# Kernel tuning notes

Hardware: AMD Instinct MI355X
Metric: run time of the kernel (lower is better)

Reference implementation:

```python
import jax, jax.numpy as jnp
import numpy as np

B, N, C, H, S = 8, 1024, 768, 8, 16  # C = 3 * S * S, head_dim = C // H
NCH = 3
D = C // H
SCALE = D ** -0.5
REATTEN_SCALE = 1.0  # transform_scale=False
EPS = 1e-5  # BatchNorm2d eps


def conv3x3(x, w, b):
    # x: (B*N, 3, S, S); w: (O=3, I=3, 3, 3) OIHW; 'same' padding
    y = jax.lax.conv_general_dilated(x, w, (1, 1), 'SAME',
                                     dimension_numbers=('NCHW', 'OIHW', 'NCHW'))
    return y + b[None, :, None, None]


def setup_inputs() -> dict:
    key = jax.random.key(0)
    ks = jax.random.split(key, 8)
    return {
        'x': jax.random.normal(ks[0], (B, N, C), jnp.float32),
        'qw': jax.random.normal(ks[1], (NCH, NCH, 3, 3), jnp.float32) * 0.1,
        'qb': jnp.zeros((NCH,), jnp.float32),
        'kw': jax.random.normal(ks[2], (NCH, NCH, 3, 3), jnp.float32) * 0.1,
        'kb': jnp.zeros((NCH,), jnp.float32),
        'vw': jax.random.normal(ks[3], (NCH, NCH, 3, 3), jnp.float32) * 0.1,
        'vb': jnp.zeros((NCH,), jnp.float32),
        'rw': jax.random.normal(ks[4], (H, H), jnp.float32) * 0.2,  # 1x1 conv over heads
        'rb': jnp.zeros((H,), jnp.float32),
        'bn_g': jnp.ones((H,), jnp.float32),
        'bn_b': jnp.zeros((H,), jnp.float32),
        'bn_m': jnp.zeros((H,), jnp.float32),   # running mean
        'bn_v': jnp.ones((H,), jnp.float32),    # running var
        'pw': jax.random.normal(ks[5], (C, C), jnp.float32) * 0.02,
        'pb': jnp.zeros((C,), jnp.float32),
    }


def reference(x, qw, qb, kw, kb, vw, vb, rw, rb, bn_g, bn_b, bn_m, bn_v, pw, pb):
    Bx, Nx, Cx = x.shape
    xs = x.reshape(Bx * Nx, NCH, S, S)  # unflatten; all (b, n) convs batched at once

    def heads(y):  # (B*N, 3, S, S) -> (B, H, N, D)
        return y.reshape(Bx, Nx, H, D).transpose(0, 2, 1, 3)

    q = heads(conv3x3(xs, qw, qb))
    k = heads(conv3x3(xs, kw, kb))
    v = heads(conv3x3(xs, vw, vb))

    attn = jnp.einsum('bhnd,bhmd->bhnm', q, k) * SCALE  # (B, H, N, N)
    attn = jax.nn.softmax(attn, axis=-1)
    # re-attention: 1x1 conv across heads, then BatchNorm2d (eval, running stats)
    attn = jnp.einsum('oh,bhnm->bonm', rw, attn) + rb[None, :, None, None]
    inv = (bn_g / jnp.sqrt(bn_v + EPS))[None, :, None, None]
    attn = (attn - bn_m[None, :, None, None]) * inv + bn_b[None, :, None, None]
    attn = attn * REATTEN_SCALE

    out = jnp.einsum('bhnm,bhmd->bhnd', attn, v)  # (B, H, N, D)
    out = out.transpose(0, 2, 1, 3).reshape(Bx, Nx, Cx)
    out = out @ pw.T + pb
    return (out, attn)
```

## Files before the change

kernel.cpp:

```cpp
#include <hip/hip_runtime.h>
#include <math.h>

#define B_ 8
#define N_ 1024
#define C_ 768
#define H_ 8
#define D_ 96
#define SCALE_F 0.1020620726159657f

typedef unsigned short u16;
typedef __bf16 bf16x8 __attribute__((ext_vector_type(8)));
typedef float f32x4 __attribute__((ext_vector_type(4)));

#define MFMA(a, b, c) __builtin_amdgcn_mfma_f32_16x16x32_bf16(a, b, c, 0, 0, 0)

__device__ inline void split1(float x, u16& h, u16& l) {
    __bf16 hb = (__bf16)x;
    float hf = (float)hb;
    __bf16 lb = (__bf16)(x - hf);
    h = __builtin_bit_cast(u16, hb);
    l = __builtin_bit_cast(u16, lb);
}

__device__ inline void split4(float4 x, ushort4& h, ushort4& l) {
    split1(x.x, h.x, l.x);
    split1(x.y, h.y, l.y);
    split1(x.z, h.z, l.z);
    split1(x.w, h.w, l.w);
}

__device__ inline void bar_lds() {
    asm volatile("s_waitcnt lgkmcnt(0)" ::: "memory");
    __builtin_amdgcn_s_barrier();
}

__global__ __launch_bounds__(256) void conv_qkv(
    const float* __restrict__ x,
    const float* __restrict__ qw, const float* __restrict__ qb,
    const float* __restrict__ kw, const float* __restrict__ kb,
    const float* __restrict__ vw, const float* __restrict__ vb,
    u16* __restrict__ qh, u16* __restrict__ ql,
    u16* __restrict__ kh, u16* __restrict__ kl,
    float* __restrict__ v)
{
    __shared__ float simg[768];
    __shared__ float sw[243];
    __shared__ float sb[9];
    const int img = blockIdx.x;
    const int b = img >> 10;
    const int tid = threadIdx.x;

    for (int i = tid; i < 768; i += 256) simg[i] = x[(size_t)img * 768 + i];
    if (tid < 243) {
        int g = tid / 81, i = tid % 81;
        const float* w = (g == 0) ? qw : (g == 1) ? kw : vw;
        sw[tid] = w[i];
    }
    if (tid < 9) {
        int g = tid / 3, i = tid % 3;
        const float* bb = (g == 0) ? qb : (g == 1) ? kb : vb;
        sb[tid] = bb[i];
    }
    __syncthreads();

    const int n = img & 1023;
    for (int e = tid; e < 2304; e += 256) {
        int g = e / 768, c = e % 768;
        int oc = c >> 8, rem = c & 255, y = rem >> 4, xx = rem & 15;
        float acc = sb[g * 3 + oc];
        const float* wg = &sw[g * 81 + oc * 27];
        #pragma unroll
        for (int ic = 0; ic < 3; ++ic)
            #pragma unroll
            for (int ky = 0; ky < 3; ++ky) {
                int yy = y + ky - 1;
                if (yy < 0 || yy > 15) continue;
                #pragma unroll
                for (int kx = 0; kx < 3; ++kx) {
                    int xp = xx + kx - 1;
                    if (xp < 0 || xp > 15) continue;
                    acc += wg[ic * 9 + ky * 3 + kx] * simg[ic * 256 + yy * 16 + xp];
                }
            }
        int hh = c / 96, d = c % 96;
        size_t o = ((size_t)(b * 8 + hh) * 1024 + n) * 96 + d;
        if (g == 2) {
            v[o] = acc;
        } else {
            u16 hi, lo;
            split1(acc, hi, lo);
            if (g == 0) { qh[o] = hi; ql[o] = lo; }
            else        { kh[o] = hi; kl[o] = lo; }
        }
    }
}

__global__ __launch_bounds__(256) void vt_split(
    const float* __restrict__ v, u16* __restrict__ vt_h)
{
    __shared__ float t32[32][36];
    const int bh = blockIdx.z, n0 = blockIdx.x * 32, d0 = blockIdx.y * 32;
    const int tid = threadIdx.x;
    {
        int nn = tid >> 3, c4 = (tid & 7) * 4;
        float4 x = *(const float4*)&v[((size_t)bh * 1024 + n0 + nn) * 96 + d0 + c4];
        t32[nn][c4] = x.x; t32[nn][c4 + 1] = x.y;
        t32[nn][c4 + 2] = x.z; t32[nn][c4 + 3] = x.w;
    }
    __syncthreads();
    {
        int d = tid >> 3, n4 = (tid & 7) * 4;
        ushort4 h;
        h.x = __builtin_bit_cast(u16, (__bf16)t32[n4][d]);
        h.y = __builtin_bit_cast(u16, (__bf16)t32[n4 + 1][d]);
        h.z = __builtin_bit_cast(u16, (__bf16)t32[n4 + 2][d]);
        h.w = __builtin_bit_cast(u16, (__bf16)t32[n4 + 3][d]);
        size_t o = ((size_t)bh * 96 + d0 + d) * 1024 + n0 + n4;
        *(ushort4*)&vt_h[o] = h;
    }
}

__global__ __launch_bounds__(256) void pw_split(
    const float* __restrict__ pw, u16* __restrict__ pwh, u16* __restrict__ pwl)
{
    int i = blockIdx.x * 256 + threadIdx.x;
    float4 x = *(const float4*)&pw[(size_t)i * 4];
    ushort4 h, l;
    split4(x, h, l);
    *(ushort4*)&pwh[(size_t)i * 4] = h;
    *(ushort4*)&pwl[(size_t)i * 4] = l;
}

__global__ __launch_bounds__(512) void fused_attn(
    const u16* __restrict__ qh, const u16* __restrict__ ql,
    const u16* __restrict__ kh, const u16* __restrict__ kl,
    const u16* __restrict__ vth,
    const float* __restrict__ rw, const float* __restrict__ rb,
    const float* __restrict__ bn_g, const float* __restrict__ bn_b,
    const float* __restrict__ bn_m, const float* __restrict__ bn_v,
    float* __restrict__ attn, u16* __restrict__ o1h, u16* __restrict__ o1l)
{
    __shared__ float p_lds[2][8][32][36];
    __shared__ float s_w2[8][8];
    __shared__ float s_b2[8];

    const int bid = blockIdx.x;
    const int b = bid & 7;
    const int n0 = (bid >> 3) * 32;
    const int tid = threadIdx.x, wid = tid >> 6, lane = tid & 63;
    const int l16 = lane & 15, kg = lane >> 4;
    const int h = wid;
    const size_t bh = (size_t)(b * 8 + h);

    if (tid < 64) {
        int o = tid >> 3, hh = tid & 7;
        float inv = bn_g[o] * rsqrtf(bn_v[o] + 1e-5f);
        s_w2[o][hh] = rw[o * 8 + hh] * inv;
        if (hh == 0) s_b2[o] = (rb[o] - bn_m[o]) * inv + bn_b[o];
    }

    bf16x8 qhf[2][3], qlf[2][3];
    #pragma unroll
    for (int nf = 0; nf < 2; ++nf)
        #pragma unroll
        for (int ks = 0; ks < 3; ++ks) {
            size_t off = (bh * 1024 + n0 + nf * 16 + l16) * 96 + ks * 32 + kg * 8;
            qhf[nf][ks] = *(const bf16x8*)&qh[off];
            qlf[nf][ks] = *(const bf16x8*)&ql[off];
        }

    float ls[2][4];
    #pragma unroll
    for (int nf = 0; nf < 2; ++nf)
        #pragma unroll
        for (int r = 0; r < 4; ++r) ls[nf][r] = 0.f;

    #pragma unroll 1
    for (int mt = 0; mt < 16; ++mt) {
        const int m0 = mt * 64;
        f32x4 sacc[2][4];
        #pragma unroll
        for (int nf = 0; nf < 2; ++nf)
            #pragma unroll
            for (int mf = 0; mf < 4; ++mf) sacc[nf][mf] = (f32x4){0.f, 0.f, 0.f, 0.f};

        __builtin_amdgcn_s_setprio(1);
        #pragma unroll
        for (int ks = 0; ks < 3; ++ks) {
            bf16x8 kbh[4];
            #pragma unroll
            for (int mf = 0; mf < 4; ++mf) {
                size_t off = (bh * 1024 + m0 + mf * 16 + l16) * 96 + ks * 32 + kg * 8;
                kbh[mf] = *(const bf16x8*)&kh[off];
            }
            #pragma unroll
            for (int nf = 0; nf < 2; ++nf)
                #pragma unroll
                for (int mf = 0; mf < 4; ++mf)
                    sacc[nf][mf] = MFMA(qhf[nf][ks], kbh[mf], sacc[nf][mf]);
        }
        __builtin_amdgcn_s_setprio(0);

        #pragma unroll
        for (int nf = 0; nf < 2; ++nf)
            #pragma unroll
            for (int mf = 0; mf < 4; ++mf)
                #pragma unroll
                for (int r = 0; r < 4; ++r)
                    ls[nf][r] += __expf(sacc[nf][mf][r] * SCALE_F);
    }

    float rv[2][4];
    #pragma unroll
    for (int nf = 0; nf < 2; ++nf)
        #pragma unroll
        for (int r = 0; r < 4; ++r) {
            float s = ls[nf][r];
            #pragma unroll
            for (int off = 1; off < 16; off <<= 1) s += __shfl_xor(s, off);
            rv[nf][r] = 1.0f / s;
        }

    __syncthreads();

    float w2r[8];
    #pragma unroll
    for (int hh = 0; hh < 8; ++hh) w2r[hh] = s_w2[h][hh];
    const float b2h = s_b2[h];

    f32x4 pvacc[2][6];
    #pragma unroll
    for (int nf = 0; nf < 2; ++nf)
        #pragma unroll
        for (int df = 0; df < 6; ++df) pvacc[nf][df] = (f32x4){0.f, 0.f, 0.f, 0.f};

#define QKEXP(MT, BUF)                                                          \
    {                                                                           \
        const int m0_ = (MT) * 32;                                              \
        f32x4 sacc_[2][2];                                                      \
        _Pragma("unroll")                                                       \
        for (int nf_ = 0; nf_ < 2; ++nf_)                                       \
            _Pragma("unroll")                                                   \
            for (int mf_ = 0; mf_ < 2; ++mf_)                                   \
                sacc_[nf_][mf_] = (f32x4){0.f, 0.f, 0.f, 0.f};                  \
        __builtin_amdgcn_s_setprio(1);                                          \
        _Pragma("unroll")                                                       \
        for (int ks_ = 0; ks_ < 3; ++ks_) {                                     \
            bf16x8 kbh_[2], kbl_[2];                                            \
            _Pragma("unroll")                                                   \
            for (int mf_ = 0; mf_ < 2; ++mf_) {                                 \
                size_t off_ = (bh * 1024 + m0_ + mf_ * 16 + l16) * 96 + ks_ * 32 + kg * 8; \
                kbh_[mf_] = *(const bf16x8*)&kh[off_];                          \
                kbl_[mf_] = *(const bf16x8*)&kl[off_];                          \
            }                                                                   \
            _Pragma("unroll")                                                   \
            for (int nf_ = 0; nf_ < 2; ++nf_)                                   \
                _Pragma("unroll")                                               \
                for (int mf_ = 0; mf_ < 2; ++mf_) {                             \
                    sacc_[nf_][mf_] = MFMA(qhf[nf_][ks_], kbh_[mf_], sacc_[nf_][mf_]); \
                    sacc_[nf_][mf_] = MFMA(qhf[nf_][ks_], kbl_[mf_], sacc_[nf_][mf_]); \
                    sacc_[nf_][mf_] = MFMA(qlf[nf_][ks_], kbh_[mf_], sacc_[nf_][mf_]); \
                }                                                               \
        }                                                                       \
        __builtin_amdgcn_s_setprio(0);                                          \
        _Pragma("unroll")                                                       \
        for (int nf_ = 0; nf_ < 2; ++nf_)                                       \
            _Pragma("unroll")                                                   \
            for (int mf_ = 0; mf_ < 2; ++mf_)                                   \
                _Pragma("unroll")                                               \
                for (int r_ = 0; r_ < 4; ++r_) {                                \
                    float pp_ = __expf(sacc_[nf_][mf_][r_] * SCALE_F) * rv[nf_][r_]; \
                    p_lds[BUF][h][nf_ * 16 + kg * 4 + r_][mf_ * 16 + l16] = pp_; \
                }                                                               \
    }

    QKEXP(0, 0)
    bar_lds();

    #pragma unroll 1
    for (int mt = 0; mt < 32; ++mt) {
        const int m0 = mt * 32;
        const int buf = mt & 1;

        bf16x8 vbh[6];
        #pragma unroll
        for (int df = 0; df < 6; ++df) {
            size_t off = (bh * 96 + df * 16 + l16) * 1024 + m0 + kg * 8;
            vbh[df] = *(const bf16x8*)&vth[off];
        }

        if (mt < 31) QKEXP(mt + 1, buf ^ 1)

        float mixf[2][8];
        #pragma unroll
        for (int nf = 0; nf < 2; ++nf)
            #pragma unroll
            for (int j = 0; j < 8; ++j) mixf[nf][j] = b2h;
        #pragma unroll
        for (int hh = 0; hh < 8; ++hh) {
            float w = w2r[hh];
            #pragma unroll
            for (int nf = 0; nf < 2; ++nf) {
                const float* pp = &p_lds[buf][hh][nf * 16 + l16][kg * 8];
                float4 a0 = *(const float4*)pp;
                float4 a1 = *(const float4*)(pp + 4);
                mixf[nf][0] += w * a0.x; mixf[nf][1] += w * a0.y;
                mixf[nf][2] += w * a0.z; mixf[nf][3] += w * a0.w;
                mixf[nf][4] += w * a1.x; mixf[nf][5] += w * a1.y;
                mixf[nf][6] += w * a1.z; mixf[nf][7] += w * a1.w;
            }
        }

        #pragma unroll
        for (int nf = 0; nf < 2; ++nf) {
            float* gp = &attn[(bh * 1024 + n0 + nf * 16 + l16) * 1024 + m0 + kg * 8];
            f32x4 v0 = {mixf[nf][0], mixf[nf][1], mixf[nf][2], mixf[nf][3]};
            f32x4 v1 = {mixf[nf][4], mixf[nf][5], mixf[nf][6], mixf[nf][7]};
            __builtin_nontemporal_store(v0, (f32x4*)gp);
            __builtin_nontemporal_store(v1, (f32x4*)(gp + 4));
        }

        bf16x8 mah[2];
        #pragma unroll
        for (int nf = 0; nf < 2; ++nf)
            #pragma unroll
            for (int j = 0; j < 8; ++j)
                mah[nf][j] = (__bf16)mixf[nf][j];
        __builtin_amdgcn_s_setprio(1);
        #pragma unroll
        for (int df = 0; df < 6; ++df)
            #pragma unroll
            for (int nf = 0; nf < 2; ++nf)
                pvacc[nf][df] = MFMA(mah[nf], vbh[df], pvacc[nf][df]);
        __builtin_amdgcn_s_setprio(0);

        bar_lds();
    }
#undef QKEXP

    #pragma unroll
    for (int nf = 0; nf < 2; ++nf)
        #pragma unroll
        for (int df = 0; df < 6; ++df)
            #pragma unroll
            for (int r = 0; r < 4; ++r) {
                int row = n0 + nf * 16 + kg * 4 + r;
                int col = h * 96 + df * 16 + l16;
                u16 hh2, ll2;
                split1(pvacc[nf][df][r], hh2, ll2);
                size_t o = ((size_t)b * 1024 + row) * 768 + col;
                o1h[o] = hh2;
                o1l[o] = ll2;
            }
}

__global__ __launch_bounds__(256) void proj_mfma(
    const u16* __restrict__ o1h, const u16* __restrict__ o1l,
    const u16* __restrict__ pwh, const u16* __restrict__ pwl,
    const float* __restrict__ pb, float* __restrict__ out)
{
    __shared__ __align__(16) u16 Ahs[5120], Als[5120];
    __shared__ __align__(16) u16 Bhs[2560], Bls[2560];
    const int t0 = blockIdx.y * 128, o0 = blockIdx.x * 64;
    const int tid = threadIdx.x;
    const int wid = tid >> 6, lane = tid & 63;
    const int l16 = lane & 15, kg = lane >> 4;
    const int wr = wid >> 1, wc = wid & 1;

    f32x4 acc[4][2];
    #pragma unroll
    for (int i = 0; i < 4; ++i)
        #pragma unroll
        for (int j = 0; j < 2; ++j) acc[i][j] = (f32x4){0.f, 0.f, 0.f, 0.f};

    for (int s = 0; s < 24; ++s) {
        const int kc = s * 32;
        if (s) __syncthreads();
        #pragma unroll
        for (int i = 0; i < 4; ++i) {
            int idx = tid + i * 256;
            int r = idx >> 3, c4 = idx & 7;
            *(ushort4*)&Ahs[r * 40 + c4 * 4] = *(const ushort4*)&o1h[(size_t)(t0 + r) * 768 + kc + c4 * 4];
            *(ushort4*)&Als[r * 40 + c4 * 4] = *(const ushort4*)&o1l[(size_t)(t0 + r) * 768 + kc + c4 * 4];
        }
        #pragma unroll
        for (int i = 0; i < 2; ++i) {
            int idx = tid + i * 256;
            int r = idx >> 3, c4 = idx & 7;
            *(ushort4*)&Bhs[r * 40 + c4 * 4] = *(const ushort4*)&pwh[(size_t)(o0 + r) * 768 + kc + c4 * 4];
            *(ushort4*)&Bls[r * 40 + c4 * 4] = *(const ushort4*)&pwl[(size_t)(o0 + r) * 768 + kc + c4 * 4];
        }
        __syncthreads();

        bf16x8 ah[4], al[4], bh8[2], bl8[2];
        #pragma unroll
        for (int f = 0; f < 4; ++f) {
            int ra = (wr * 64 + f * 16 + l16) * 40 + kg * 8;
            ah[f] = *(const bf16x8*)&Ahs[ra];
            al[f] = *(const bf16x8*)&Als[ra];
        }
        #pragma unroll
        for (int j = 0; j < 2; ++j) {
            int rb = (wc * 32 + j * 16 + l16) * 40 + kg * 8;
            bh8[j] = *(const bf16x8*)&Bhs[rb];
            bl8[j] = *(const bf16x8*)&Bls[rb];
        }
        #pragma unroll
        for (int i = 0; i < 4; ++i)
            #pragma unroll
            for (int j = 0; j < 2; ++j) {
                acc[i][j] = MFMA(ah[i], bh8[j], acc[i][j]);
                acc[i][j] = MFMA(ah[i], bl8[j], acc[i][j]);
                acc[i][j] = MFMA(al[i], bh8[j], acc[i][j]);
            }
    }

    #pragma unroll
    for (int i = 0; i < 4; ++i) {
        int rr = t0 + wr * 64 + i * 16 + kg * 4;
        #pragma unroll
        for (int j = 0; j < 2; ++j) {
            int cc = o0 + wc * 32 + j * 16 + l16;
            float bias = pb[cc];
            #pragma unroll
            for (int r = 0; r < 4; ++r)
                __builtin_nontemporal_store(acc[i][j][r] + bias,
                                            &out[(size_t)(rr + r) * 768 + cc]);
        }
    }
}

extern "C" void kernel_launch(void* const* d_in, const int* in_sizes, int n_in,
                              void* d_out, int out_size, void* d_ws, size_t ws_size,
                              hipStream_t stream)
{
    const float* x    = (const float*)d_in[0];
    const float* qw   = (const float*)d_in[1];
    const float* qb   = (const float*)d_in[2];
    const float* kw   = (const float*)d_in[3];
    const float* kb   = (const float*)d_in[4];
    const float* vw   = (const float*)d_in[5];
    const float* vb   = (const float*)d_in[6];
    const float* rw   = (const float*)d_in[7];
    const float* rb   = (const float*)d_in[8];
    const float* bn_g = (const float*)d_in[9];
    const float* bn_b = (const float*)d_in[10];
    const float* bn_m = (const float*)d_in[11];
    const float* bn_v = (const float*)d_in[12];
    const float* pw   = (const float*)d_in[13];
    const float* pb   = (const float*)d_in[14];

    float* out_p  = (float*)d_out;
    float* attn_p = out_p + (size_t)B_ * N_ * C_;

    float* ws = (float*)d_ws;
    const size_t qkv = (size_t)B_ * H_ * N_ * D_;

    float* vf  = ws;
    u16* qhp = (u16*)(ws + qkv);
    u16* qlp = qhp + qkv;
    u16* khp = qlp + qkv;
    u16* klp = khp + qkv;
    u16* vth = (u16*)(ws + 3 * qkv);
    u16* o1h = (u16*)(ws + 4 * qkv);
    u16* o1l = o1h + qkv;
    u16* pwh = (u16*)(ws + 5 * qkv);
    u16* pwl = pwh + (size_t)C_ * C_;

    conv_qkv<<<B_ * N_, 256, 0, stream>>>(x, qw, qb, kw, kb, vw, vb,
                                          qhp, qlp, khp, klp, vf);
    vt_split<<<dim3(32, 3, 64), 256, 0, stream>>>(vf, vth);
    pw_split<<<576, 256, 0, stream>>>(pw, pwh, pwl);
    fused_attn<<<256, 512, 0, stream>>>(qhp, qlp, khp, klp, vth,
                                        rw, rb, bn_g, bn_b, bn_m, bn_v,
                                        attn_p, o1h, o1l);
    proj_mfma<<<dim3(12, 64), 256, 0, stream>>>(o1h, o1l, pwh, pwl, pb, out_p);
}
```

Baseline: 294.6 us.

## Compute head-mixing once per element via bf16 head-interleaved LDS staging

Softmax probabilities are now staged in LDS as bf16 with the head index innermost. Each thread reads all 8 heads for one (n,m) position and computes all 8 mixed output heads, so each wave no longer rereads every head's 32x32 tile. The mixed values are written to the attention output with coalesced scalar stores and staged through a second bf16 LDS buffer for the PV MFMA, using a mid-iteration barrier. This cuts redundant LDS reads and halves LDS footprint per element. In exchange, probabilities are rounded to bf16 before mixing, which lowers the precision of the returned attention map, and global stores are narrower.

```diff
diff --git a/kernel.cpp b/kernel.cpp
--- a/kernel.cpp
+++ b/kernel.cpp
@@ -11,6 +11,7 @@
 typedef unsigned short u16;
 typedef __bf16 bf16x8 __attribute__((ext_vector_type(8)));
 typedef float f32x4 __attribute__((ext_vector_type(4)));
+typedef u16 u16x8 __attribute__((ext_vector_type(8)));
 
 #define MFMA(a, b, c) __builtin_amdgcn_mfma_f32_16x16x32_bf16(a, b, c, 0, 0, 0)
 
@@ -32,6 +33,10 @@
 __device__ inline void bar_lds() {
     asm volatile("s_waitcnt lgkmcnt(0)" ::: "memory");
     __builtin_amdgcn_s_barrier();
+}
+
+__device__ inline float bf16_to_f32(u16 u) {
+    return __builtin_bit_cast(float, (unsigned)u << 16);
 }
 
 __global__ __launch_bounds__(256) void conv_qkv(
@@ -140,7 +145,8 @@
     const float* __restrict__ bn_m, const float* __restrict__ bn_v,
     float* __restrict__ attn, u16* __restrict__ o1h, u16* __restrict__ o1l)
 {
-    __shared__ float p_lds[2][8][32][36];
+    __shared__ u16 p_lds[2][32][33][8];
+    __shared__ u16 m_lds[2][8][32][40];
     __shared__ float s_w2[8][8];
     __shared__ float s_b2[8];
 
@@ -223,16 +229,23 @@
 
     __syncthreads();
 
-    float w2r[8];
-    #pragma unroll
-    for (int hh = 0; hh < 8; ++hh) w2r[hh] = s_w2[h][hh];
-    const float b2h = s_b2[h];
+    float w2all[8][8], b2r[8];
+    #pragma unroll
+    for (int o = 0; o < 8; ++o) {
+        b2r[o] = s_b2[o];
+        #pragma unroll
+        for (int hh = 0; hh < 8; ++hh) w2all[o][hh] = s_w2[o][hh];
+    }
 
     f32x4 pvacc[2][6];
     #pragma unroll
     for (int nf = 0; nf < 2; ++nf)
         #pragma unroll
         for (int df = 0; df < 6; ++df) pvacc[nf][df] = (f32x4){0.f, 0.f, 0.f, 0.f};
+
+    const int mm = lane & 31, halfq = lane >> 5;
+    const int nlA = wid * 4 + halfq;
+    const int nlB = wid * 4 + 2 + halfq;
 
 #define QKEXP(MT, BUF)                                                          \
     {                                                                           \
@@ -270,7 +283,8 @@
                 _Pragma("unroll")                                               \
                 for (int r_ = 0; r_ < 4; ++r_) {                                \
                     float pp_ = __expf(sacc_[nf_][mf_][r_] * SCALE_F) * rv[nf_][r_]; \
-                    p_lds[BUF][h][nf_ * 16 + kg * 4 + r_][mf_ * 16 + l16] = pp_; \
+                    p_lds[BUF][nf_ * 16 + kg * 4 + r_][mf_ * 16 + l16][h] =     \
+                        __builtin_bit_cast(u16, (__bf16)pp_);                   \
                 }                                                               \
     }
 
@@ -291,41 +305,41 @@
 
         if (mt < 31) QKEXP(mt + 1, buf ^ 1)
 
-        float mixf[2][8];
+        {
+            u16x8 pa = *(const u16x8*)&p_lds[buf][nlA][mm][0];
+            u16x8 pb = *(const u16x8*)&p_lds[buf][nlB][mm][0];
+            float macc[2][8];
+            #pragma unroll
+            for (int o = 0; o < 8; ++o) { macc[0][o] = b2r[o]; macc[1][o] = b2r[o]; }
+            #pragma unroll
+            for (int hh = 0; hh < 8; ++hh) {
+                float pA = bf16_to_f32(pa[hh]);
+                float pB = bf16_to_f32(pb[hh]);
+                #pragma unroll
+                for (int o = 0; o < 8; ++o) {
+                    macc[0][o] += w2all[o][hh] * pA;
+                    macc[1][o] += w2all[o][hh] * pB;
+                }
+            }
+            #pragma unroll
+            for (int o = 0; o < 8; ++o) {
+                size_t basео = ((size_t)(b * 8 + o) * 1024 + n0);
+                __builtin_nontemporal_store(macc[0][o],
+                    &attn[(basео + nlA) * 1024 + m0 + mm]);
+                __builtin_nontemporal_store(macc[1][o],
+                    &attn[(basео + nlB) * 1024 + m0 + mm]);
+                m_lds[buf][o][nlA][mm] = __builtin_bit_cast(u16, (__bf16)macc[0][o]);
+                m_lds[buf][o][nlB][mm] = __builtin_bit_cast(u16, (__bf16)macc[1][o]);
+            }
+        }
+
+        bar_lds();
+
+        bf16x8 mah[2];
         #pragma unroll
         for (int nf = 0; nf < 2; ++nf)
-            #pragma unroll
-            for (int j = 0; j < 8; ++j) mixf[nf][j] = b2h;
-        #pragma unroll
-        for (int hh = 0; hh < 8; ++hh) {
-            float w = w2r[hh];
-            #pragma unroll
-            for (int nf = 0; nf < 2; ++nf) {
-                const float* pp = &p_lds[buf][hh][nf * 16 + l16][kg * 8];
-                float4 a0 = *(const float4*)pp;
-                float4 a1 = *(const float4*)(pp + 4);
-                mixf[nf][0] += w * a0.x; mixf[nf][1] += w * a0.y;
-                mixf[nf][2] += w * a0.z; mixf[nf][3] += w * a0.w;
-                mixf[nf][4] += w * a1.x; mixf[nf][5] += w * a1.y;
-                mixf[nf][6] += w * a1.z; mixf[nf][7] += w * a1.w;
-            }
-        }
-
-        #pragma unroll
-        for (int nf = 0; nf < 2; ++nf) {
-            float* gp = &attn[(bh * 1024 + n0 + nf * 16 + l16) * 1024 + m0 + kg * 8];
-            f32x4 v0 = {mixf[nf][0], mixf[nf][1], mixf[nf][2], mixf[nf][3]};
-            f32x4 v1 = {mixf[nf][4], mixf[nf][5], mixf[nf][6], mixf[nf][7]};
-            __builtin_nontemporal_store(v0, (f32x4*)gp);
-            __builtin_nontemporal_store(v1, (f32x4*)(gp + 4));
-        }
-
-        bf16x8 mah[2];
-        #pragma unroll
-        for (int nf = 0; nf < 2; ++nf)
-            #pragma unroll
-            for (int j = 0; j < 8; ++j)
-                mah[nf][j] = (__bf16)mixf[nf][j];
+            mah[nf] = __builtin_bit_cast(bf16x8,
+                *(const u16x8*)&m_lds[buf][wid][nf * 16 + l16][kg * 8]);
         __builtin_amdgcn_s_setprio(1);
         #pragma unroll
         for (int df = 0; df < 6; ++df)
@@ -333,8 +347,6 @@
             for (int nf = 0; nf < 2; ++nf)
                 pvacc[nf][df] = MFMA(mah[nf], vbh[df], pvacc[nf][df]);
         __builtin_amdgcn_s_setprio(0);
-
-        bar_lds();
     }
 #undef QKEXP
 
```

Result: slower. 324.4 us (+10.1%).

## Split attention over key halves and move softmax stats to separate kernel

Applied to the files above, without the earlier changes.

Moves the row-sum (softmax denominator) pass into its own qk_stats kernel and splits the fused attention kernel over two halves of the key dimension, doubling the grid to 512 blocks. Each half writes fp32 partial outputs, which a new merge kernel sums and splits into bf16 hi/lo for the projection. The aim is to fill more compute units than the previous one-block-per-CU grid. In exchange it adds two kernel launches and extra global memory traffic for the fp32 partials.

```diff
diff --git a/kernel.cpp b/kernel.cpp
--- a/kernel.cpp
+++ b/kernel.cpp
@@ -131,14 +131,70 @@
     *(ushort4*)&pwl[(size_t)i * 4] = l;
 }
 
+__global__ __launch_bounds__(512) void qk_stats(
+    const u16* __restrict__ qh, const u16* __restrict__ kh,
+    float* __restrict__ srv)
+{
+    const int bid = blockIdx.x;
+    const int b = bid & 7;
+    const int n0 = (bid >> 3) * 16;
+    const int tid = threadIdx.x, wid = tid >> 6, lane = tid & 63;
+    const int l16 = lane & 15, kg = lane >> 4;
+    const size_t bh = (size_t)(b * 8 + wid);
+
+    bf16x8 qhf[3];
+    #pragma unroll
+    for (int ks = 0; ks < 3; ++ks)
+        qhf[ks] = *(const bf16x8*)&qh[(bh * 1024 + n0 + l16) * 96 + ks * 32 + kg * 8];
+
+    float ls[4] = {0.f, 0.f, 0.f, 0.f};
+
+    #pragma unroll 1
+    for (int mt = 0; mt < 16; ++mt) {
+        const int m0 = mt * 64;
+        f32x4 sacc[4];
+        #pragma unroll
+        for (int mf = 0; mf < 4; ++mf) sacc[mf] = (f32x4){0.f, 0.f, 0.f, 0.f};
+
+        __builtin_amdgcn_s_setprio(1);
+        #pragma unroll
+        for (int ks = 0; ks < 3; ++ks) {
+            bf16x8 kbh[4];
+            #pragma unroll
+            for (int mf = 0; mf < 4; ++mf)
+                kbh[mf] = *(const bf16x8*)&kh[(bh * 1024 + m0 + mf * 16 + l16) * 96 + ks * 32 + kg * 8];
+            #pragma unroll
+            for (int mf = 0; mf < 4; ++mf)
+                sacc[mf] = MFMA(qhf[ks], kbh[mf], sacc[mf]);
+        }
+        __builtin_amdgcn_s_setprio(0);
+
+        #pragma unroll
+        for (int mf = 0; mf < 4; ++mf)
+            #pragma unroll
+            for (int r = 0; r < 4; ++r)
+                ls[r] += __expf(sacc[mf][r] * SCALE_F);
+    }
+
+    #pragma unroll
+    for (int r = 0; r < 4; ++r) {
+        float s = ls[r];
+        #pragma unroll
+        for (int off = 1; off < 16; off <<= 1) s += __shfl_xor(s, off);
+        if (l16 == 0)
+            srv[bh * 1024 + n0 + kg * 4 + r] = 1.0f / s;
+    }
+}
+
 __global__ __launch_bounds__(512) void fused_attn(
     const u16* __restrict__ qh, const u16* __restrict__ ql,
     const u16* __restrict__ kh, const u16* __restrict__ kl,
-    const u16* __restrict__ vth,
+    const u16* __restrict__ vth, const float* __restrict__ srv,
     const float* __restrict__ rw, const float* __restrict__ rb,
     const float* __restrict__ bn_g, const float* __restrict__ bn_b,
     const float* __restrict__ bn_m, const float* __restrict__ bn_v,
-    float* __restrict__ attn, u16* __restrict__ o1h, u16* __restrict__ o1l)
+    float* __restrict__ attn,
+    float* __restrict__ o1p0, float* __restrict__ o1p1)
 {
     __shared__ float p_lds[2][8][32][36];
     __shared__ float s_w2[8][8];
@@ -146,7 +202,11 @@
 
     const int bid = blockIdx.x;
     const int b = bid & 7;
-    const int n0 = (bid >> 3) * 32;
+    const int n0 = ((bid >> 3) & 31) * 32;
+    const int mhalf = bid >> 8;
+    const int mbase = mhalf * 512;
+    float* __restrict__ o1p = mhalf ? o1p1 : o1p0;
+
     const int tid = threadIdx.x, wid = tid >> 6, lane = tid & 63;
     const int l16 = lane & 15, kg = lane >> 4;
     const int h = wid;
@@ -169,57 +229,12 @@
             qlf[nf][ks] = *(const bf16x8*)&ql[off];
         }
 
-    float ls[2][4];
+    float rv[2][4];
     #pragma unroll
     for (int nf = 0; nf < 2; ++nf)
         #pragma unroll
-        for (int r = 0; r < 4; ++r) ls[nf][r] = 0.f;
-
-    #pragma unroll 1
-    for (int mt = 0; mt < 16; ++mt) {
-        const int m0 = mt * 64;
-        f32x4 sacc[2][4];
-        #pragma unroll
-        for (int nf = 0; nf < 2; ++nf)
-            #pragma unroll
-            for (int mf = 0; mf < 4; ++mf) sacc[nf][mf] = (f32x4){0.f, 0.f, 0.f, 0.f};
-
-        __builtin_amdgcn_s_setprio(1);
-        #pragma unroll
-        for (int ks = 0; ks < 3; ++ks) {
-            bf16x8 kbh[4];
-            #pragma unroll
-            for (int mf = 0; mf < 4; ++mf) {
-                size_t off = (bh * 1024 + m0 + mf * 16 + l16) * 96 + ks * 32 + kg * 8;
-                kbh[mf] = *(const bf16x8*)&kh[off];
-            }
-            #pragma unroll
-            for (int nf = 0; nf < 2; ++nf)
-                #pragma unroll
-                for (int mf = 0; mf < 4; ++mf)
-                    sacc[nf][mf] = MFMA(qhf[nf][ks], kbh[mf], sacc[nf][mf]);
-        }
-        __builtin_amdgcn_s_setprio(0);
-
-        #pragma unroll
-        for (int nf = 0; nf < 2; ++nf)
-            #pragma unroll
-            for (int mf = 0; mf < 4; ++mf)
-                #pragma unroll
-                for (int r = 0; r < 4; ++r)
-                    ls[nf][r] += __expf(sacc[nf][mf][r] * SCALE_F);
-    }
-
-    float rv[2][4];
-    #pragma unroll
-    for (int nf = 0; nf < 2; ++nf)
-        #pragma unroll
-        for (int r = 0; r < 4; ++r) {
-            float s = ls[nf][r];
-            #pragma unroll
-            for (int off = 1; off < 16; off <<= 1) s += __shfl_xor(s, off);
-            rv[nf][r] = 1.0f / s;
-        }
+        for (int r = 0; r < 4; ++r)
+            rv[nf][r] = srv[bh * 1024 + n0 + nf * 16 + kg * 4 + r];
 
     __syncthreads();
 
@@ -236,7 +251,7 @@
 
 #define QKEXP(MT, BUF)                                                          \
     {                                                                           \
-        const int m0_ = (MT) * 32;                                              \
+        const int m0_ = mbase + (MT) * 32;                                      \
         f32x4 sacc_[2][2];                                                      \
         _Pragma("unroll")                                                       \
         for (int nf_ = 0; nf_ < 2; ++nf_)                                       \
@@ -278,8 +293,8 @@
     bar_lds();
 
     #pragma unroll 1
-    for (int mt = 0; mt < 32; ++mt) {
-        const int m0 = mt * 32;
+    for (int mt = 0; mt < 16; ++mt) {
+        const int m0 = mbase + mt * 32;
         const int buf = mt & 1;
 
         bf16x8 vbh[6];
@@ -289,7 +304,7 @@
             vbh[df] = *(const bf16x8*)&vth[off];
         }
 
-        if (mt < 31) QKEXP(mt + 1, buf ^ 1)
+        if (mt < 15) QKEXP(mt + 1, buf ^ 1)
 
         float mixf[2][8];
         #pragma unroll
@@ -346,12 +361,23 @@
             for (int r = 0; r < 4; ++r) {
                 int row = n0 + nf * 16 + kg * 4 + r;
                 int col = h * 96 + df * 16 + l16;
-                u16 hh2, ll2;
-                split1(pvacc[nf][df][r], hh2, ll2);
-                size_t o = ((size_t)b * 1024 + row) * 768 + col;
-                o1h[o] = hh2;
-                o1l[o] = ll2;
+                __builtin_nontemporal_store(pvacc[nf][df][r],
+                    &o1p[((size_t)b * 1024 + row) * 768 + col]);
             }
+}
+
+__global__ __launch_bounds__(256) void merge_o1(
+    const float* __restrict__ p0, const float* __restrict__ p1,
+    u16* __restrict__ o1h, u16* __restrict__ o1l)
+{
+    size_t i = ((size_t)blockIdx.x * 256 + threadIdx.x) * 4;
+    float4 a = *(const float4*)&p0[i];
+    float4 c = *(const float4*)&p1[i];
+    a.x += c.x; a.y += c.y; a.z += c.z; a.w += c.w;
+    ushort4 h, l;
+    split4(a, h, l);
+    *(ushort4*)&o1h[i] = h;
+    *(ushort4*)&o1l[i] = l;
 }
 
 __global__ __launch_bounds__(256) void proj_mfma(
@@ -462,17 +488,22 @@
     u16* khp = qlp + qkv;
     u16* klp = khp + qkv;
     u16* vth = (u16*)(ws + 3 * qkv);
-    u16* o1h = (u16*)(ws + 4 * qkv);
+    u16* o1h = (u16*)(ws + 3 * qkv + qkv / 2);
     u16* o1l = o1h + qkv;
-    u16* pwh = (u16*)(ws + 5 * qkv);
+    u16* pwh = (u16*)(ws + 4 * qkv + qkv / 2);
     u16* pwl = pwh + (size_t)C_ * C_;
+    float* srv = ws + 4 * qkv + qkv / 2 + 589824;
+    float* o1p0 = vf;
+    float* o1p1 = ws + 5 * qkv;
 
     conv_qkv<<<B_ * N_, 256, 0, stream>>>(x, qw, qb, kw, kb, vw, vb,
                                           qhp, qlp, khp, klp, vf);
     vt_split<<<dim3(32, 3, 64), 256, 0, stream>>>(vf, vth);
     pw_split<<<576, 256, 0, stream>>>(pw, pwh, pwl);
-    fused_attn<<<256, 512, 0, stream>>>(qhp, qlp, khp, klp, vth,
+    qk_stats<<<512, 512, 0, stream>>>(qhp, khp, srv);
+    fused_attn<<<512, 512, 0, stream>>>(qhp, qlp, khp, klp, vth, srv,
                                         rw, rb, bn_g, bn_b, bn_m, bn_v,
-                                        attn_p, o1h, o1l);
+                                        attn_p, o1p0, o1p1);
+    merge_o1<<<6144, 256, 0, stream>>>(o1p0, o1p1, o1h, o1l);
     proj_mfma<<<dim3(12, 64), 256, 0, stream>>>(o1h, o1l, pwh, pwl, pb, out_p);
 }
```

New measurement: 365.6 us. 1.24x slower.

## Split attention PV over key halves with 1024-thread blocks and merge kernel

Applied to the files above, without the earlier changes.

Each fused_attn block now covers 64 query rows instead of 32, run by two 8-wave groups, and only half of the key range. Each block writes fp32 partial P·V results to one of two buffers, and a new merge_o1 kernel sums them and does the bf16 hi/lo split. The aim is to double resident waves per CU so latency is better hidden. In exchange, the row-sum pass over all keys is repeated by both key halves, fp32 partials add extra memory traffic plus a launch, and a 1024-thread limit may squeeze registers.

```diff
diff --git a/kernel.cpp b/kernel.cpp
--- a/kernel.cpp
+++ b/kernel.cpp
@@ -131,25 +131,31 @@
     *(ushort4*)&pwl[(size_t)i * 4] = l;
 }
 
-__global__ __launch_bounds__(512) void fused_attn(
+__global__ __launch_bounds__(1024) void fused_attn(
     const u16* __restrict__ qh, const u16* __restrict__ ql,
     const u16* __restrict__ kh, const u16* __restrict__ kl,
     const u16* __restrict__ vth,
     const float* __restrict__ rw, const float* __restrict__ rb,
     const float* __restrict__ bn_g, const float* __restrict__ bn_b,
     const float* __restrict__ bn_m, const float* __restrict__ bn_v,
-    float* __restrict__ attn, u16* __restrict__ o1h, u16* __restrict__ o1l)
-{
-    __shared__ float p_lds[2][8][32][36];
+    float* __restrict__ attn,
+    float* __restrict__ o1p0, float* __restrict__ o1p1)
+{
+    __shared__ float p_lds[2][2][8][32][36];
     __shared__ float s_w2[8][8];
     __shared__ float s_b2[8];
 
     const int bid = blockIdx.x;
     const int b = bid & 7;
-    const int n0 = (bid >> 3) * 32;
+    const int n0 = ((bid >> 3) & 15) * 64;
+    const int mhalf = bid >> 7;
+    const int mbase = mhalf * 512;
+    float* __restrict__ o1p = mhalf ? o1p1 : o1p0;
+
     const int tid = threadIdx.x, wid = tid >> 6, lane = tid & 63;
+    const int grp = wid >> 3, h = wid & 7;
     const int l16 = lane & 15, kg = lane >> 4;
-    const int h = wid;
+    const int nb = n0 + grp * 32;
     const size_t bh = (size_t)(b * 8 + h);
 
     if (tid < 64) {
@@ -164,7 +170,7 @@
     for (int nf = 0; nf < 2; ++nf)
         #pragma unroll
         for (int ks = 0; ks < 3; ++ks) {
-            size_t off = (bh * 1024 + n0 + nf * 16 + l16) * 96 + ks * 32 + kg * 8;
+            size_t off = (bh * 1024 + nb + nf * 16 + l16) * 96 + ks * 32 + kg * 8;
             qhf[nf][ks] = *(const bf16x8*)&qh[off];
             qlf[nf][ks] = *(const bf16x8*)&ql[off];
         }
@@ -236,7 +242,7 @@
 
 #define QKEXP(MT, BUF)                                                          \
     {                                                                           \
-        const int m0_ = (MT) * 32;                                              \
+        const int m0_ = mbase + (MT) * 32;                                      \
         f32x4 sacc_[2][2];                                                      \
         _Pragma("unroll")                                                       \
         for (int nf_ = 0; nf_ < 2; ++nf_)                                       \
@@ -270,7 +276,7 @@
                 _Pragma("unroll")                                               \
                 for (int r_ = 0; r_ < 4; ++r_) {                                \
                     float pp_ = __expf(sacc_[nf_][mf_][r_] * SCALE_F) * rv[nf_][r_]; \
-                    p_lds[BUF][h][nf_ * 16 + kg * 4 + r_][mf_ * 16 + l16] = pp_; \
+                    p_lds[BUF][grp][h][nf_ * 16 + kg * 4 + r_][mf_ * 16 + l16] = pp_; \
                 }                                                               \
     }
 
@@ -278,8 +284,8 @@
     bar_lds();
 
     #pragma unroll 1
-    for (int mt = 0; mt < 32; ++mt) {
-        const int m0 = mt * 32;
+    for (int mt = 0; mt < 16; ++mt) {
+        const int m0 = mbase + mt * 32;
         const int buf = mt & 1;
 
         bf16x8 vbh[6];
@@ -289,7 +295,7 @@
             vbh[df] = *(const bf16x8*)&vth[off];
         }
 
-        if (mt < 31) QKEXP(mt + 1, buf ^ 1)
+        if (mt < 15) QKEXP(mt + 1, buf ^ 1)
 
         float mixf[2][8];
         #pragma unroll
@@ -301,7 +307,7 @@
             float w = w2r[hh];
             #pragma unroll
             for (int nf = 0; nf < 2; ++nf) {
-                const float* pp = &p_lds[buf][hh][nf * 16 + l16][kg * 8];
+                const float* pp = &p_lds[buf][grp][hh][nf * 16 + l16][kg * 8];
                 float4 a0 = *(const float4*)pp;
                 float4 a1 = *(const float4*)(pp + 4);
                 mixf[nf][0] += w * a0.x; mixf[nf][1] += w * a0.y;
@@ -313,7 +319,7 @@
 
         #pragma unroll
         for (int nf = 0; nf < 2; ++nf) {
-            float* gp = &attn[(bh * 1024 + n0 + nf * 16 + l16) * 1024 + m0 + kg * 8];
+            float* gp = &attn[(bh * 1024 + nb + nf * 16 + l16) * 1024 + m0 + kg * 8];
             f32x4 v0 = {mixf[nf][0], mixf[nf][1], mixf[nf][2], mixf[nf][3]};
             f32x4 v1 = {mixf[nf][4], mixf[nf][5], mixf[nf][6], mixf[nf][7]};
             __builtin_nontemporal_store(v0, (f32x4*)gp);
@@ -344,14 +350,25 @@
         for (int df = 0; df < 6; ++df)
             #pragma unroll
             for (int r = 0; r < 4; ++r) {
-                int row = n0 + nf * 16 + kg * 4 + r;
+                int row = nb + nf * 16 + kg * 4 + r;
                 int col = h * 96 + df * 16 + l16;
-                u16 hh2, ll2;
-                split1(pvacc[nf][df][r], hh2, ll2);
-                size_t o = ((size_t)b * 1024 + row) * 768 + col;
-                o1h[o] = hh2;
-                o1l[o] = ll2;
+                __builtin_nontemporal_store(pvacc[nf][df][r],
+                    &o1p[((size_t)b * 1024 + row) * 768 + col]);
             }
+}
+
+__global__ __launch_bounds__(256) void merge_o1(
+    const float* __restrict__ p0, const float* __restrict__ p1,
+    u16* __restrict__ o1h, u16* __restrict__ o1l)
+{
+    size_t i = ((size_t)blockIdx.x * 256 + threadIdx.x) * 4;
+    float4 a = *(const float4*)&p0[i];
+    float4 c = *(const float4*)&p1[i];
+    a.x += c.x; a.y += c.y; a.z += c.z; a.w += c.w;
+    ushort4 h, l;
+    split4(a, h, l);
+    *(ushort4*)&o1h[i] = h;
+    *(ushort4*)&o1l[i] = l;
 }
 
 __global__ __launch_bounds__(256) void proj_mfma(
@@ -462,17 +479,20 @@
     u16* khp = qlp + qkv;
     u16* klp = khp + qkv;
     u16* vth = (u16*)(ws + 3 * qkv);
-    u16* o1h = (u16*)(ws + 4 * qkv);
+    u16* o1h = (u16*)(ws + 3 * qkv + qkv / 2);
     u16* o1l = o1h + qkv;
-    u16* pwh = (u16*)(ws + 5 * qkv);
+    u16* pwh = (u16*)(ws + 4 * qkv + qkv / 2);
     u16* pwl = pwh + (size_t)C_ * C_;
+    float* o1p0 = vf;
+    float* o1p1 = ws + 5 * qkv;
 
     conv_qkv<<<B_ * N_, 256, 0, stream>>>(x, qw, qb, kw, kb, vw, vb,
                                           qhp, qlp, khp, klp, vf);
     vt_split<<<dim3(32, 3, 64), 256, 0, stream>>>(vf, vth);
     pw_split<<<576, 256, 0, stream>>>(pw, pwh, pwl);
-    fused_attn<<<256, 512, 0, stream>>>(qhp, qlp, khp, klp, vth,
-                                        rw, rb, bn_g, bn_b, bn_m, bn_v,
-                                        attn_p, o1h, o1l);
+    fused_attn<<<256, 1024, 0, stream>>>(qhp, qlp, khp, klp, vth,
+                                         rw, rb, bn_g, bn_b, bn_m, bn_v,
+                                         attn_p, o1p0, o1p1);
+    merge_o1<<<6144, 256, 0, stream>>>(o1p0, o1p1, o1h, o1l);
     proj_mfma<<<dim3(12, 64), 256, 0, stream>>>(o1h, o1l, pwh, pwl, pb, out_p);
 }
```

After: 527.3 us. 79.0% more time.
